# Performance work log

Hardware: AMD Instinct MI355X
Metric: run time of the kernel (lower is better)

The kernel has to match this reference:

```python
import jax, jax.numpy as jnp
import numpy as np

N = 50000
E = 800000
IN_C = 256
OUT_C = 256
HEADS = 8
HEAD_C = OUT_C // HEADS  # 32
BNECK = OUT_C // 4       # 64
NEG_SLOPE = 0.2
BN_EPS = 1e-5


def _bn(x, gamma, beta):
    # BatchNorm1d over node dim, batch statistics (deterministic train-mode math)
    mu = jnp.mean(x, axis=0)
    var = jnp.var(x, axis=0)
    return (x - mu) * jax.lax.rsqrt(var + BN_EPS) * gamma + beta


def setup_inputs() -> dict:
    key = jax.random.key(0)
    ks = jax.random.split(key, 16)
    s = lambda fan: 1.0 / np.sqrt(fan)
    x = jax.random.normal(ks[0], (N, IN_C), dtype=jnp.float32)
    edge_index = jax.random.randint(ks[1], (2, E), 0, N, dtype=jnp.int64)
    return {
        "x": x,
        "edge_index": edge_index,
        # GATConv params (lin has no bias in PyG)
        "W_lin": jax.random.normal(ks[2], (IN_C, HEADS * HEAD_C), jnp.float32) * s(IN_C),
        "att_src": jax.random.normal(ks[3], (HEADS, HEAD_C), jnp.float32) * s(HEAD_C),
        "att_dst": jax.random.normal(ks[4], (HEADS, HEAD_C), jnp.float32) * s(HEAD_C),
        "conv_bias": jnp.zeros((HEADS * HEAD_C,), jnp.float32),
        "W_res": jax.random.normal(ks[5], (IN_C, HEADS * HEAD_C), jnp.float32) * s(IN_C),
        # gnn.BatchNorm
        "g_norm": jnp.ones((OUT_C,), jnp.float32),
        "b_norm": jnp.zeros((OUT_C,), jnp.float32),
        # Bottleneck down
        "W_down": jax.random.normal(ks[6], (OUT_C, BNECK), jnp.float32) * s(OUT_C),
        "b_down": jnp.zeros((BNECK,), jnp.float32),
        "g_down": jnp.ones((BNECK,), jnp.float32),
        "bb_down": jnp.zeros((BNECK,), jnp.float32),
        # Bottleneck up
        "W_up": jax.random.normal(ks[7], (BNECK, OUT_C), jnp.float32) * s(BNECK),
        "b_up": jnp.zeros((OUT_C,), jnp.float32),
        "g_up": jnp.ones((OUT_C,), jnp.float32),
        "bb_up": jnp.zeros((OUT_C,), jnp.float32),
    }


def _forward(x, edge_index, W_lin, att_src, att_dst, conv_bias, W_res,
             g_norm, b_norm, W_down, b_down, g_down, bb_down,
             W_up, b_up, g_up, bb_up):
    src, dst = edge_index[0], edge_index[1]
    # --- GATConv ---
    xh = (x @ W_lin).reshape(N, HEADS, HEAD_C)            # [N,H,C]
    a_src = jnp.einsum("nhc,hc->nh", xh, att_src)          # [N,H]
    a_dst = jnp.einsum("nhc,hc->nh", xh, att_dst)          # [N,H]
    e = a_src[src] + a_dst[dst]                             # [E,H]
    e = jnp.where(e > 0, e, NEG_SLOPE * e)                  # leaky_relu
    # segment softmax over destination nodes (numerically stable)
    m = jax.ops.segment_max(e, dst, num_segments=N)         # [N,H]
    m = jnp.where(jnp.isfinite(m), m, 0.0)
    ex = jnp.exp(e - m[dst])
    denom = jax.ops.segment_sum(ex, dst, num_segments=N)    # [N,H]
    alpha = ex / (denom[dst] + 1e-16)                        # [E,H]
    msgs = xh[src] * alpha[:, :, None]                       # [E,H,C]
    out = jax.ops.segment_sum(msgs, dst, num_segments=N)    # [N,H,C]
    out = out.reshape(N, HEADS * HEAD_C) + conv_bias + x @ W_res  # GAT residual + bias
    # --- norm + act ---
    h = jax.nn.elu(_bn(out, g_norm, b_norm))
    # --- bottleneck ---
    d = jax.nn.elu(_bn(h @ W_down + b_down, g_down, bb_down))
    u = jax.nn.elu(_bn(d @ W_up + b_up, g_up, bb_up))
    h = h + u
    # dropout: eval mode (identity); in==out so identity skip
    return h + x


def reference(x, edge_index, W_lin, att_src, att_dst, conv_bias, W_res,
              g_norm, b_norm, W_down, b_down, g_down, bb_down,
              W_up, b_up, g_up, bb_up):
    return _forward(x, edge_index, W_lin, att_src, att_dst, conv_bias, W_res,
                    g_norm, b_norm, W_down, b_down, g_down, bb_down,
                    W_up, b_up, g_up, bb_up)
```

## Files before the change

### kernel.cpp

```cpp
#include <hip/hip_runtime.h>

#define NN 50000
#define EE 800000
#define HEADS 8
#define NEG 0.2f
#define BN_EPS 1e-5f
#define SCAN_B 196

typedef unsigned int uint;
typedef unsigned short ushort;

typedef __bf16 bf16x8 __attribute__((ext_vector_type(8)));
typedef float f32x4 __attribute__((ext_vector_type(4)));

__device__ __forceinline__ float bflo(uint u) { return __uint_as_float(u << 16); }
__device__ __forceinline__ float bfhi(uint u) { return __uint_as_float(u & 0xffff0000u); }
__device__ __forceinline__ float bf1(ushort u) { return __uint_as_float(((uint)u) << 16); }
__device__ __forceinline__ ushort f2bf(float f) {
  uint u = __float_as_uint(f);
  u += 0x7fff + ((u >> 16) & 1);
  return (ushort)(u >> 16);
}
__device__ __forceinline__ uint pk2(float a, float b) {
  return (uint)f2bf(a) | ((uint)f2bf(b) << 16);
}
__device__ __forceinline__ float eluf(float v) { return v > 0.f ? v : expm1f(v); }

__device__ __forceinline__ int blk_detect_bf16(const uint* __restrict__ xw) {
  __shared__ int s_bf;
  int t = threadIdx.x;
  if (t < 64) {
    int good = 0;
#pragma unroll
    for (int j = 0; j < 4; ++j) {
      uint lo = xw[t * 4 + j] & 0xffffu;
      uint ex = (lo >> 7) & 0xffu;
      good += (ex >= 110u && ex <= 140u) ? 1 : 0;
    }
    for (int o = 32; o; o >>= 1) good += __shfl_down(good, o);
    if (t == 0) s_bf = (good >= 128) ? 1 : 0;
  }
  __syncthreads();
  return s_bf;
}

__device__ __forceinline__ int blk_detect_i64(const int* __restrict__ ew) {
  __shared__ int s_i64;
  int t = threadIdx.x;
  if (t < 64) {
    int zeros = 0;
#pragma unroll
    for (int j = 0; j < 4; ++j)
      zeros += (ew[2 * (t * 4 + j) + 1] == 0) ? 1 : 0;
    for (int o = 32; o; o >>= 1) zeros += __shfl_down(zeros, o);
    if (t == 0) s_i64 = (zeros >= 200) ? 1 : 0;
  }
  __syncthreads();
  return s_i64;
}

__global__ __launch_bounds__(256)
void k_prep(const void* __restrict__ x,
            const void* p0, const void* p1, const void* p2, const void* p3,
            const void* p4, const void* p5, const void* p6, const void* p7,
            const void* p8, const void* p9, const void* p10,
            const void* W_lin, const void* W_res, const void* W_down, const void* W_up,
            float* __restrict__ P, ushort* __restrict__ bt1,
            ushort* __restrict__ bt2, ushort* __restrict__ bt3) {
  __shared__ ushort tile[64][65];
  int bf = blk_detect_bf16((const uint*)x);
  int b = blockIdx.x, t = threadIdx.x;
  if (b < 11) {
    const void* srcs[11] = {p0, p1, p2, p3, p4, p5, p6, p7, p8, p9, p10};
    const int sz[11]  = {256, 256, 256, 256, 256, 64, 64, 64, 256, 256, 256};
    const int off[11] = {0, 256, 512, 768, 1024, 1280, 1344, 1408, 1472, 1728, 1984};
    if (t < sz[b]) {
      const void* s = srcs[b];
      P[off[b] + t] = bf ? bf1(((const ushort*)s)[t]) : ((const float*)s)[t];
    }
    return;
  }
  const void* src; ushort* dst; int R, C, D, rb, cb;
  if (b < 27)      { int u = b - 11; src = W_lin;  dst = bt1;         R = 256; C = 256; D = 256; rb = u & 3; cb = u >> 2; }
  else if (b < 43) { int u = b - 27; src = W_res;  dst = bt1 + 65536; R = 256; C = 256; D = 256; rb = u & 3; cb = u >> 2; }
  else if (b < 51) { int u = b - 43; src = W_down; dst = bt2;         R = 256; C = 64;  D = 128; rb = u & 3; cb = u >> 2; }
  else             { int u = b - 51; src = W_up;   dst = bt3;         R = 64;  C = 256; D = 256; rb = 0;     cb = u; }
  int r0 = rb * 64, c0 = cb * 64;
  int tr = t >> 6, tc = t & 63;
#pragma unroll
  for (int i = 0; i < 16; ++i) {
    int rl = tr + i * 4;
    int r = r0 + rl, c = c0 + tc;
    float v = 0.f;
    if (r < R && c < C)
      v = bf ? bf1(((const ushort*)src)[(size_t)r * C + c])
             : ((const float*)src)[(size_t)r * C + c];
    tile[rl][tc] = f2bf(v);
  }
  __syncthreads();
#pragma unroll
  for (int i = 0; i < 16; ++i) {
    int cl = tr + i * 4;
    int rl = tc;
    int c = c0 + cl, r = r0 + rl;
    if (c < D && r < R)
      dst[(size_t)c * R + r] = (c < C) ? tile[rl][cl] : (ushort)0;
  }
}

__global__ __launch_bounds__(256)
void k_edges(const int* __restrict__ raw, int* __restrict__ sc, int* __restrict__ dc,
             int* __restrict__ count) {
  int i64 = blk_detect_i64(raw);
  int e = blockIdx.x * 256 + threadIdx.x;
  if (e >= EE) return;
  int s, d;
  if (i64) { s = raw[2 * e]; d = raw[2 * (EE + e)]; }
  else     { s = raw[e];     d = raw[EE + e]; }
  if ((uint)s >= NN) s = 0;
  if ((uint)d >= NN) d = 0;
  sc[e] = s; dc[e] = d;
  atomicAdd(&count[d], 1);
}

__global__ __launch_bounds__(256)
void k_gemm(const void* __restrict__ A, const ushort* __restrict__ Bt,
            int aMode, int nIter, int M, int K, int mode,
            ushort* __restrict__ o_xh, ushort* __restrict__ o_xres,
            ushort* __restrict__ o_bf, int NC, const float* __restrict__ bias,
            const float* __restrict__ bnsums, const float* __restrict__ bng,
            const float* __restrict__ bnb) {
  __shared__ __align__(16) ushort As[128 * 32];
  __shared__ __align__(16) ushort Bs[128 * 32];
  __shared__ float scs[256], shs[256];
  int t = threadIdx.x;
  int l = t & 63, w = t >> 6;
  int wr = w >> 1, wc = w & 1;
  int lr = l & 15, lq = l >> 4;
  int m0 = blockIdx.x * 128;
  const ushort* Ab = (const ushort*)A;
  const float*  Af = (const float*)A;

  int af32 = 0;
  if (aMode == 1) af32 = blk_detect_bf16((const uint*)A) ? 0 : 1;
  if (aMode == 2) {
    if (t < K) {
      const float invN = 1.0f / NN;
      float mean = bnsums[t] * invN;
      float var = bnsums[K + t] * invN - mean * mean;
      float sc = bng[t] * rsqrtf(var + BN_EPS);
      scs[t] = sc;
      shs[t] = bnb[t] - mean * sc;
    }
  }

  for (int nc = 0; nc < nIter; ++nc) {
    int n0 = nc * 128;
    f32x4 acc[4][4];
#pragma unroll
    for (int i = 0; i < 4; ++i)
#pragma unroll
      for (int j = 0; j < 4; ++j) acc[i][j] = (f32x4){0.f, 0.f, 0.f, 0.f};

    for (int kt = 0; kt < K; kt += 32) {
      __syncthreads();
#pragma unroll
      for (int r = 0; r < 2; ++r) {
        int ci = r * 256 + t;
        int m = ci >> 2, ko = (ci & 3) << 3;
        int gm = m0 + m; gm = gm < M ? gm : M - 1;
        if (aMode == 1 && af32) {
          float4 u0 = *(const float4*)(Af + (size_t)gm * K + kt + ko);
          float4 u1 = *(const float4*)(Af + (size_t)gm * K + kt + ko + 4);
          uint4 o;
          o.x = pk2(u0.x, u0.y); o.y = pk2(u0.z, u0.w);
          o.z = pk2(u1.x, u1.y); o.w = pk2(u1.z, u1.w);
          *(uint4*)(&As[m * 32 + ko]) = o;
        } else if (aMode == 2) {
          uint4 q = *(const uint4*)(Ab + (size_t)gm * K + kt + ko);
          int cb = kt + ko;
          float v0 = eluf(bflo(q.x) * scs[cb + 0] + shs[cb + 0]);
          float v1 = eluf(bfhi(q.x) * scs[cb + 1] + shs[cb + 1]);
          float v2 = eluf(bflo(q.y) * scs[cb + 2] + shs[cb + 2]);
          float v3 = eluf(bfhi(q.y) * scs[cb + 3] + shs[cb + 3]);
          float v4 = eluf(bflo(q.z) * scs[cb + 4] + shs[cb + 4]);
          float v5 = eluf(bfhi(q.z) * scs[cb + 5] + shs[cb + 5]);
          float v6 = eluf(bflo(q.w) * scs[cb + 6] + shs[cb + 6]);
          float v7 = eluf(bfhi(q.w) * scs[cb + 7] + shs[cb + 7]);
          uint4 o;
          o.x = pk2(v0, v1); o.y = pk2(v2, v3);
          o.z = pk2(v4, v5); o.w = pk2(v6, v7);
          *(uint4*)(&As[m * 32 + ko]) = o;
        } else {
          *(uint4*)(&As[m * 32 + ko]) = *(const uint4*)(Ab + (size_t)gm * K + kt + ko);
        }
        *(uint4*)(&Bs[m * 32 + ko]) = *(const uint4*)(Bt + (size_t)(n0 + m) * K + kt + ko);
      }
      __syncthreads();
      bf16x8 af[4], bf[4];
#pragma unroll
      for (int i = 0; i < 4; ++i) {
        af[i] = *(const bf16x8*)(&As[(wr * 64 + i * 16 + lr) * 32 + lq * 8]);
        bf[i] = *(const bf16x8*)(&Bs[(wc * 64 + i * 16 + lr) * 32 + lq * 8]);
      }
#pragma unroll
      for (int i = 0; i < 4; ++i)
#pragma unroll
        for (int j = 0; j < 4; ++j)
          acc[i][j] = __builtin_amdgcn_mfma_f32_16x16x32_bf16(af[i], bf[j], acc[i][j], 0, 0, 0);
    }

#pragma unroll
    for (int i = 0; i < 4; ++i) {
      int gr0 = m0 + wr * 64 + i * 16 + lq * 4;
#pragma unroll
      for (int j = 0; j < 4; ++j) {
        int gc = n0 + wc * 64 + j * 16 + lr;
#pragma unroll
        for (int r = 0; r < 4; ++r) {
          int row = gr0 + r;
          if (row >= M) continue;
          float v = acc[i][j][r];
          if (mode == 0) {
            if (gc < 256) o_xh[(size_t)row * 256 + gc] = f2bf(v);
            else          o_xres[(size_t)row * 256 + (gc - 256)] = f2bf(v);
          } else {
            if (gc < NC) o_bf[(size_t)row * NC + gc] = f2bf(v + bias[gc]);
          }
        }
      }
    }
  }
}

__global__ void k_attn(const ushort* __restrict__ xh, const float* __restrict__ P,
                       float* __restrict__ a_src, float* __restrict__ a_dst) {
  int id = blockIdx.x * 256 + threadIdx.x;
  if (id >= NN * HEADS) return;
  int n = id >> 3, h = id & 7;
  const uint4* xr = (const uint4*)(xh + (size_t)n * 256 + h * 32);
  const float4* pa = (const float4*)(P + h * 32);
  const float4* pd = (const float4*)(P + 256 + h * 32);
  float s = 0.f, d = 0.f;
#pragma unroll
  for (int j = 0; j < 4; ++j) {
    uint4 q = xr[j];
    float4 a0 = pa[2 * j], a1 = pa[2 * j + 1];
    float4 d0 = pd[2 * j], d1 = pd[2 * j + 1];
    float x0 = bflo(q.x), x1 = bfhi(q.x), x2 = bflo(q.y), x3 = bfhi(q.y);
    float x4 = bflo(q.z), x5 = bfhi(q.z), x6 = bflo(q.w), x7 = bfhi(q.w);
    s += x0 * a0.x + x1 * a0.y + x2 * a0.z + x3 * a0.w
       + x4 * a1.x + x5 * a1.y + x6 * a1.z + x7 * a1.w;
    d += x0 * d0.x + x1 * d0.y + x2 * d0.z + x3 * d0.w
       + x4 * d1.x + x5 * d1.y + x6 * d1.z + x7 * d1.w;
  }
  a_src[id] = s; a_dst[id] = d;
}

__global__ void k_scan_bs(const int* __restrict__ count, int* __restrict__ bsum) {
  __shared__ int s[256];
  int i = blockIdx.x * 256 + threadIdx.x;
  s[threadIdx.x] = (i < NN) ? count[i] : 0;
  __syncthreads();
  for (int off = 128; off > 0; off >>= 1) {
    if (threadIdx.x < off) s[threadIdx.x] += s[threadIdx.x + off];
    __syncthreads();
  }
  if (threadIdx.x == 0) bsum[blockIdx.x] = s[0];
}

__global__ void k_scan_top(const int* __restrict__ bsum, int* __restrict__ boff,
                           int* __restrict__ rowptr) {
  __shared__ int s[256];
  int t = threadIdx.x;
  int v = (t < SCAN_B) ? bsum[t] : 0;
  s[t] = v;
  __syncthreads();
  for (int off = 1; off < 256; off <<= 1) {
    int u = (t >= off) ? s[t - off] : 0;
    __syncthreads();
    s[t] += u;
    __syncthreads();
  }
  boff[t] = s[t] - v;
  if (t == 255) rowptr[NN] = s[255];
}

__global__ void k_scan_wr(const int* __restrict__ count, const int* __restrict__ boff,
                          int* __restrict__ rowptr, int* __restrict__ rowwork) {
  __shared__ int s[256];
  int b = blockIdx.x, t = threadIdx.x;
  int i = b * 256 + t;
  int v = (i < NN) ? count[i] : 0;
  s[t] = v;
  __syncthreads();
  for (int off = 1; off < 256; off <<= 1) {
    int u = (t >= off) ? s[t - off] : 0;
    __syncthreads();
    s[t] += u;
    __syncthreads();
  }
  if (i < NN) {
    int ex = boff[b] + s[t] - v;
    rowptr[i] = ex;
    rowwork[i] = ex;
  }
}

__global__ void k_scatter(const int* __restrict__ sc, const int* __restrict__ dc,
                          int* __restrict__ rowwork, int* __restrict__ perm_src) {
  int e = blockIdx.x * 256 + threadIdx.x;
  if (e >= EE) return;
  int pos = atomicAdd(&rowwork[dc[e]], 1);
  perm_src[pos] = sc[e];
}

__global__ __launch_bounds__(256)
void k_aggregate(const int* __restrict__ rowptr, const int* __restrict__ perm_src,
                 const float* __restrict__ a_src, const float* __restrict__ a_dst,
                 const ushort* __restrict__ xh, const ushort* __restrict__ xres,
                 const float* __restrict__ bias, ushort* __restrict__ outb) {
  int n = blockIdx.x * 4 + (threadIdx.x >> 6);
  int l = threadIdx.x & 63;
  if (n >= NN) return;
  int half = l >> 5;
  int q = l & 31;
  int h = q >> 2;
  float ad = a_dst[n * 8 + h];
  int st = rowptr[n], en = rowptr[n + 1];
  float a0 = 0.f, a1 = 0.f, a2 = 0.f, a3 = 0.f;
  float a4 = 0.f, a5 = 0.f, a6 = 0.f, a7 = 0.f, sum = 0.f;
  int p = st + half;
  int s_c = 0; float e_c = 0.f; uint4 x_c = {0, 0, 0, 0};
  if (p < en) {
    s_c = perm_src[p];
    e_c = a_src[s_c * 8 + h];
    x_c = *(const uint4*)(xh + (size_t)s_c * 256 + q * 8);
  }
  for (; p < en; p += 2) {
    int pn = p + 2;
    int s_n = 0; float e_n = 0.f; uint4 x_n = {0, 0, 0, 0};
    if (pn < en) {
      s_n = perm_src[pn];
      e_n = a_src[s_n * 8 + h];
      x_n = *(const uint4*)(xh + (size_t)s_n * 256 + q * 8);
    }
    float v = e_c + ad;
    v = v > 0.f ? v : NEG * v;
    float wgt = __expf(fminf(v, 60.f));
    sum += wgt;
    a0 += wgt * bflo(x_c.x); a1 += wgt * bfhi(x_c.x);
    a2 += wgt * bflo(x_c.y); a3 += wgt * bfhi(x_c.y);
    a4 += wgt * bflo(x_c.z); a5 += wgt * bfhi(x_c.z);
    a6 += wgt * bflo(x_c.w); a7 += wgt * bfhi(x_c.w);
    s_c = s_n; e_c = e_n; x_c = x_n;
  }
  sum += __shfl_xor(sum, 32);
  a0 += __shfl_xor(a0, 32); a1 += __shfl_xor(a1, 32);
  a2 += __shfl_xor(a2, 32); a3 += __shfl_xor(a3, 32);
  a4 += __shfl_xor(a4, 32); a5 += __shfl_xor(a5, 32);
  a6 += __shfl_xor(a6, 32); a7 += __shfl_xor(a7, 32);
  if (half == 0) {
    float inv = 1.0f / (sum + 1e-16f);
    int cb = q * 8;
    float4 b0 = *(const float4*)(bias + cb);
    float4 b1 = *(const float4*)(bias + cb + 4);
    uint4 qr = *(const uint4*)(xres + (size_t)n * 256 + cb);
    uint4 pk;
    pk.x = pk2(a0 * inv + b0.x + bflo(qr.x), a1 * inv + b0.y + bfhi(qr.x));
    pk.y = pk2(a2 * inv + b0.z + bflo(qr.y), a3 * inv + b0.w + bfhi(qr.y));
    pk.z = pk2(a4 * inv + b1.x + bflo(qr.z), a5 * inv + b1.y + bfhi(qr.z));
    pk.w = pk2(a6 * inv + b1.z + bflo(qr.w), a7 * inv + b1.w + bfhi(qr.w));
    *(uint4*)(outb + (size_t)n * 256 + cb) = pk;
  }
}

__global__ __launch_bounds__(256)
void k_stats_p(const ushort* __restrict__ x, float* __restrict__ sums, int n, int C) {
  __shared__ float4 redA[256];
  __shared__ float4 redB[256];
  int t = threadIdx.x, b = blockIdx.x;
  int W = C >> 2;
  int c4 = t & (W - 1);
  int rl = t / W;
  int G = 256 / W;
  int rows = (n + 63) / 64;
  int r0 = b * rows, r1 = r0 + rows; if (r1 > n) r1 = n;
  const uint2* xu = (const uint2*)x;
  float s0 = 0, s1 = 0, s2 = 0, s3 = 0, q0 = 0, q1 = 0, q2 = 0, q3 = 0;
  for (int r = r0 + rl; r < r1; r += G) {
    uint2 v = xu[(size_t)r * W + c4];
    float v0 = bflo(v.x), v1 = bfhi(v.x), v2 = bflo(v.y), v3 = bfhi(v.y);
    s0 += v0; s1 += v1; s2 += v2; s3 += v3;
    q0 += v0 * v0; q1 += v1 * v1; q2 += v2 * v2; q3 += v3 * v3;
  }
  redA[t] = make_float4(s0, s1, s2, s3);
  redB[t] = make_float4(q0, q1, q2, q3);
  __syncthreads();
  for (int off = 128; off >= W; off >>= 1) {
    if (t < off) {
      float4 a = redA[t + off], c = redA[t];
      redA[t] = make_float4(c.x + a.x, c.y + a.y, c.z + a.z, c.w + a.w);
      float4 d = redB[t + off], e = redB[t];
      redB[t] = make_float4(e.x + d.x, e.y + d.y, e.z + d.z, e.w + d.w);
    }
    __syncthreads();
  }
  if (t < W) {
    float4 a = redA[t], d = redB[t];
    atomicAdd(&sums[4 * c4 + 0], a.x); atomicAdd(&sums[4 * c4 + 1], a.y);
    atomicAdd(&sums[4 * c4 + 2], a.z); atomicAdd(&sums[4 * c4 + 3], a.w);
    atomicAdd(&sums[C + 4 * c4 + 0], d.x); atomicAdd(&sums[C + 4 * c4 + 1], d.y);
    atomicAdd(&sums[C + 4 * c4 + 2], d.z); atomicAdd(&sums[C + 4 * c4 + 3], d.w);
  }
}

__global__ void k_final(const ushort* __restrict__ upre, const float* __restrict__ sums3,
                        const ushort* __restrict__ og, const float* __restrict__ sums1,
                        const float* __restrict__ P, const void* __restrict__ xsrc,
                        void* __restrict__ outv) {
  int bf = blk_detect_bf16((const uint*)xsrc);
  int id = blockIdx.x * 256 + threadIdx.x;
  size_t base = (size_t)id * 4;
  if (base >= (size_t)NN * 256) return;
  int c = (int)(base & 255);
  const float invN = 1.0f / NN;
  float4 s3m = *(const float4*)(sums3 + c);
  float4 s3q = *(const float4*)(sums3 + 256 + c);
  float4 g3 = *(const float4*)(P + 1728 + c);
  float4 b3 = *(const float4*)(P + 1984 + c);
  float4 s1m = *(const float4*)(sums1 + c);
  float4 s1q = *(const float4*)(sums1 + 256 + c);
  float4 g1 = *(const float4*)(P + 768 + c);
  float4 b1 = *(const float4*)(P + 1024 + c);
  uint2 qu = *(const uint2*)(upre + base);
  uint2 qo = *(const uint2*)(og + base);
  float xv[4];
  if (bf) {
    uint2 qx = *(const uint2*)((const ushort*)xsrc + base);
    xv[0] = bflo(qx.x); xv[1] = bfhi(qx.x); xv[2] = bflo(qx.y); xv[3] = bfhi(qx.y);
  } else {
    float4 qx = *(const float4*)((const float*)xsrc + base);
    xv[0] = qx.x; xv[1] = qx.y; xv[2] = qx.z; xv[3] = qx.w;
  }
  float uv[4] = {bflo(qu.x), bfhi(qu.x), bflo(qu.y), bfhi(qu.y)};
  float ov[4] = {bflo(qo.x), bfhi(qo.x), bflo(qo.y), bfhi(qo.y)};
  float s3mv[4] = {s3m.x, s3m.y, s3m.z, s3m.w}, s3qv[4] = {s3q.x, s3q.y, s3q.z, s3q.w};
  float g3v[4] = {g3.x, g3.y, g3.z, g3.w}, b3v[4] = {b3.x, b3.y, b3.z, b3.w};
  float s1mv[4] = {s1m.x, s1m.y, s1m.z, s1m.w}, s1qv[4] = {s1q.x, s1q.y, s1q.z, s1q.w};
  float g1v[4] = {g1.x, g1.y, g1.z, g1.w}, b1v[4] = {b1.x, b1.y, b1.z, b1.w};
  float o[4];
#pragma unroll
  for (int j = 0; j < 4; ++j) {
    float m3 = s3mv[j] * invN;
    float v3 = s3qv[j] * invN - m3 * m3;
    float sc3 = g3v[j] * rsqrtf(v3 + BN_EPS);
    float u = eluf((uv[j] - m3) * sc3 + b3v[j]);
    float m1 = s1mv[j] * invN;
    float v1 = s1qv[j] * invN - m1 * m1;
    float sc1 = g1v[j] * rsqrtf(v1 + BN_EPS);
    float h1 = eluf((ov[j] - m1) * sc1 + b1v[j]);
    o[j] = u + h1 + xv[j];
  }
  if (bf) {
    uint2 pk;
    pk.x = pk2(o[0], o[1]);
    pk.y = pk2(o[2], o[3]);
    *(uint2*)((ushort*)outv + base) = pk;
  } else {
    *(float4*)((float*)outv + base) = make_float4(o[0], o[1], o[2], o[3]);
  }
}

extern "C" void kernel_launch(void* const* d_in, const int* in_sizes, int n_in,
                              void* d_out, int out_size, void* d_ws, size_t ws_size,
                              hipStream_t stream) {
  const void* x      = d_in[0];
  const int*  ei     = (const int*)d_in[1];
  const void* W_lin  = d_in[2];
  const void* att_s  = d_in[3];
  const void* att_d  = d_in[4];
  const void* c_bias = d_in[5];
  const void* W_res  = d_in[6];
  const void* g_norm = d_in[7];
  const void* b_norm = d_in[8];
  const void* W_down = d_in[9];
  const void* b_down = d_in[10];
  const void* g_down = d_in[11];
  const void* bb_down= d_in[12];
  const void* W_up   = d_in[13];
  const void* b_up   = d_in[14];
  const void* g_up   = d_in[15];
  const void* bb_up  = d_in[16];

  char* ws = (char*)d_ws;
  size_t off = 0;
  auto alloc = [&](size_t bytes) -> char* {
    char* p = ws + off;
    off = (off + bytes + 255) & ~(size_t)255;
    return p;
  };
  int*   count  = (int*)alloc((size_t)NN * 4);
  float* sums1  = (float*)alloc(512 * 4);
  float* sums2  = (float*)alloc(128 * 4);
  float* sums3  = (float*)alloc(512 * 4);
  size_t zbytes = off;
  float* P      = (float*)alloc(2240 * 4);
  int* bsum     = (int*)alloc(256 * 4);
  int* boff     = (int*)alloc(256 * 4);
  int* rowptr   = (int*)alloc((size_t)(NN + 1) * 4);
  int* rowwork  = (int*)alloc((size_t)(NN + 1) * 4);
  int* src_c    = (int*)alloc((size_t)EE * 4);
  int* dst_c    = (int*)alloc((size_t)EE * 4);
  int* perm_src = (int*)alloc((size_t)EE * 4);
  ushort* bt1   = (ushort*)alloc((size_t)512 * 256 * 2);
  ushort* bt2   = (ushort*)alloc((size_t)128 * 256 * 2);
  ushort* bt3   = (ushort*)alloc((size_t)256 * 64 * 2);
  float* a_src  = (float*)alloc((size_t)NN * 8 * 4);
  float* a_dst  = (float*)alloc((size_t)NN * 8 * 4);
  ushort* xh    = (ushort*)alloc((size_t)NN * 256 * 2);
  ushort* xres  = (ushort*)alloc((size_t)NN * 256 * 2);
  ushort* og_b  = (ushort*)alloc((size_t)NN * 256 * 2);
  ushort* d_pre_b = xh;
  ushort* u_pre_b = xres;

  hipMemsetAsync(d_ws, 0, zbytes, stream);

  hipLaunchKernelGGL(k_prep, dim3(55), dim3(256), 0, stream, x,
                     att_s, att_d, c_bias, g_norm, b_norm, b_down, g_down, bb_down,
                     b_up, g_up, bb_up, W_lin, W_res, W_down, W_up, P, bt1, bt2, bt3);
  hipLaunchKernelGGL(k_edges, dim3((EE + 255) / 256), dim3(256), 0, stream,
                     ei, src_c, dst_c, count);

  hipLaunchKernelGGL(k_gemm, dim3(391), dim3(256), 0, stream, x, bt1, 1, 4,
                     NN, 256, 0, xh, xres, (ushort*)nullptr, 0,
                     (const float*)nullptr, (const float*)nullptr,
                     (const float*)nullptr, (const float*)nullptr);
  hipLaunchKernelGGL(k_attn, dim3((NN * 8 + 255) / 256), dim3(256), 0, stream,
                     xh, P, a_src, a_dst);

  hipLaunchKernelGGL(k_scan_bs, dim3(SCAN_B), dim3(256), 0, stream, count, bsum);
  hipLaunchKernelGGL(k_scan_top, dim3(1), dim3(256), 0, stream, bsum, boff, rowptr);
  hipLaunchKernelGGL(k_scan_wr, dim3(SCAN_B), dim3(256), 0, stream, count, boff, rowptr, rowwork);
  hipLaunchKernelGGL(k_scatter, dim3((EE + 255) / 256), dim3(256), 0, stream,
                     src_c, dst_c, rowwork, perm_src);

  hipLaunchKernelGGL(k_aggregate, dim3(NN / 4), dim3(256), 0, stream, rowptr, perm_src,
                     a_src, a_dst, xh, xres, P + 512, og_b);

  hipLaunchKernelGGL(k_stats_p, dim3(64), dim3(256), 0, stream, og_b, sums1, NN, 256);

  hipLaunchKernelGGL(k_gemm, dim3(391), dim3(256), 0, stream, og_b, bt2, 2, 1,
                     NN, 256, 1, (ushort*)nullptr, (ushort*)nullptr, d_pre_b, 64,
                     P + 1280, sums1, P + 768, P + 1024);
  hipLaunchKernelGGL(k_stats_p, dim3(64), dim3(256), 0, stream, d_pre_b, sums2, NN, 64);

  hipLaunchKernelGGL(k_gemm, dim3(391), dim3(256), 0, stream, d_pre_b, bt3, 2, 2,
                     NN, 64, 1, (ushort*)nullptr, (ushort*)nullptr, u_pre_b, 256,
                     P + 1472, sums2, P + 1344, P + 1408);
  hipLaunchKernelGGL(k_stats_p, dim3(64), dim3(256), 0, stream, u_pre_b, sums3, NN, 256);

  hipLaunchKernelGGL(k_final, dim3(NN * 256 / 4 / 256), dim3(256), 0, stream,
                     u_pre_b, sums3, og_b, sums1, P, x, d_out);
}
```

Measured before the change: 621.3 us.

## Stage full A row-tile in padded LDS once and read B directly from global

The GEMM kernel now loads the block's whole 128xK A tile into dynamic shared memory once, padded by 8 elements per row to avoid bank conflicts, with the BN+ELU prologue applied during that load. It then reuses the tile across all N-chunks instead of re-staging A for every chunk. B fragments are read straight from global memory (cached) inside the K loop, which removes the per-iteration barriers and B staging. The cost is larger LDS use (about 66 KB for K=256), which can lower occupancy, plus uncoalesced per-lane global B loads.

```diff
diff --git a/kernel.cpp b/kernel.cpp
--- a/kernel.cpp
+++ b/kernel.cpp
@@ -130,29 +130,60 @@
             ushort* __restrict__ o_bf, int NC, const float* __restrict__ bias,
             const float* __restrict__ bnsums, const float* __restrict__ bng,
             const float* __restrict__ bnb) {
-  __shared__ __align__(16) ushort As[128 * 32];
-  __shared__ __align__(16) ushort Bs[128 * 32];
+  extern __shared__ __align__(16) ushort Asl[];
   __shared__ float scs[256], shs[256];
   int t = threadIdx.x;
   int l = t & 63, w = t >> 6;
   int wr = w >> 1, wc = w & 1;
   int lr = l & 15, lq = l >> 4;
   int m0 = blockIdx.x * 128;
+  int stride = K + 8;
   const ushort* Ab = (const ushort*)A;
   const float*  Af = (const float*)A;
 
+  if (aMode == 2 && t < K) {
+    const float invN = 1.0f / NN;
+    float mean = bnsums[t] * invN;
+    float var = bnsums[K + t] * invN - mean * mean;
+    float sc = bng[t] * rsqrtf(var + BN_EPS);
+    scs[t] = sc;
+    shs[t] = bnb[t] - mean * sc;
+  }
+  __syncthreads();
   int af32 = 0;
   if (aMode == 1) af32 = blk_detect_bf16((const uint*)A) ? 0 : 1;
-  if (aMode == 2) {
-    if (t < K) {
-      const float invN = 1.0f / NN;
-      float mean = bnsums[t] * invN;
-      float var = bnsums[K + t] * invN - mean * mean;
-      float sc = bng[t] * rsqrtf(var + BN_EPS);
-      scs[t] = sc;
-      shs[t] = bnb[t] - mean * sc;
-    }
-  }
+
+  int W = K >> 3;
+  int total = 128 * W;
+  for (int ci = t; ci < total; ci += 256) {
+    int m = ci / W, ko = (ci - m * W) * 8;
+    int gm = m0 + m; gm = gm < M ? gm : M - 1;
+    uint4 o;
+    if (aMode == 1 && af32) {
+      float4 u0 = *(const float4*)(Af + (size_t)gm * K + ko);
+      float4 u1 = *(const float4*)(Af + (size_t)gm * K + ko + 4);
+      o.x = pk2(u0.x, u0.y); o.y = pk2(u0.z, u0.w);
+      o.z = pk2(u1.x, u1.y); o.w = pk2(u1.z, u1.w);
+    } else {
+      uint4 q = *(const uint4*)(Ab + (size_t)gm * K + ko);
+      if (aMode == 2) {
+        float v0 = eluf(bflo(q.x) * scs[ko + 0] + shs[ko + 0]);
+        float v1 = eluf(bfhi(q.x) * scs[ko + 1] + shs[ko + 1]);
+        float v2 = eluf(bflo(q.y) * scs[ko + 2] + shs[ko + 2]);
+        float v3 = eluf(bfhi(q.y) * scs[ko + 3] + shs[ko + 3]);
+        float v4 = eluf(bflo(q.z) * scs[ko + 4] + shs[ko + 4]);
+        float v5 = eluf(bfhi(q.z) * scs[ko + 5] + shs[ko + 5]);
+        float v6 = eluf(bflo(q.w) * scs[ko + 6] + shs[ko + 6]);
+        float v7 = eluf(bfhi(q.w) * scs[ko + 7] + shs[ko + 7]);
+        o.x = pk2(v0, v1); o.y = pk2(v2, v3);
+        o.z = pk2(v4, v5); o.w = pk2(v6, v7);
+      } else {
+        o = q;
+      }
+    }
+    *(uint4*)(&Asl[m * stride + ko]) = o;
+  }
+  __syncthreads();
 
   for (int nc = 0; nc < nIter; ++nc) {
     int n0 = nc * 128;
@@ -162,47 +193,17 @@
 #pragma unroll
       for (int j = 0; j < 4; ++j) acc[i][j] = (f32x4){0.f, 0.f, 0.f, 0.f};
 
+    const ushort* bbase = Bt + (size_t)(n0 + wc * 64 + lr) * K + lq * 8;
+    const ushort* arow = &Asl[(wr * 64 + lr) * stride + lq * 8];
+
     for (int kt = 0; kt < K; kt += 32) {
-      __syncthreads();
-#pragma unroll
-      for (int r = 0; r < 2; ++r) {
-        int ci = r * 256 + t;
-        int m = ci >> 2, ko = (ci & 3) << 3;
-        int gm = m0 + m; gm = gm < M ? gm : M - 1;
-        if (aMode == 1 && af32) {
-          float4 u0 = *(const float4*)(Af + (size_t)gm * K + kt + ko);
-          float4 u1 = *(const float4*)(Af + (size_t)gm * K + kt + ko + 4);
-          uint4 o;
-          o.x = pk2(u0.x, u0.y); o.y = pk2(u0.z, u0.w);
-          o.z = pk2(u1.x, u1.y); o.w = pk2(u1.z, u1.w);
-          *(uint4*)(&As[m * 32 + ko]) = o;
-        } else if (aMode == 2) {
-          uint4 q = *(const uint4*)(Ab + (size_t)gm * K + kt + ko);
-          int cb = kt + ko;
-          float v0 = eluf(bflo(q.x) * scs[cb + 0] + shs[cb + 0]);
-          float v1 = eluf(bfhi(q.x) * scs[cb + 1] + shs[cb + 1]);
-          float v2 = eluf(bflo(q.y) * scs[cb + 2] + shs[cb + 2]);
-          float v3 = eluf(bfhi(q.y) * scs[cb + 3] + shs[cb + 3]);
-          float v4 = eluf(bflo(q.z) * scs[cb + 4] + shs[cb + 4]);
-          float v5 = eluf(bfhi(q.z) * scs[cb + 5] + shs[cb + 5]);
-          float v6 = eluf(bflo(q.w) * scs[cb + 6] + shs[cb + 6]);
-          float v7 = eluf(bfhi(q.w) * scs[cb + 7] + shs[cb + 7]);
-          uint4 o;
-          o.x = pk2(v0, v1); o.y = pk2(v2, v3);
-          o.z = pk2(v4, v5); o.w = pk2(v6, v7);
-          *(uint4*)(&As[m * 32 + ko]) = o;
-        } else {
-          *(uint4*)(&As[m * 32 + ko]) = *(const uint4*)(Ab + (size_t)gm * K + kt + ko);
-        }
-        *(uint4*)(&Bs[m * 32 + ko]) = *(const uint4*)(Bt + (size_t)(n0 + m) * K + kt + ko);
-      }
-      __syncthreads();
       bf16x8 af[4], bf[4];
 #pragma unroll
-      for (int i = 0; i < 4; ++i) {
-        af[i] = *(const bf16x8*)(&As[(wr * 64 + i * 16 + lr) * 32 + lq * 8]);
-        bf[i] = *(const bf16x8*)(&Bs[(wc * 64 + i * 16 + lr) * 32 + lq * 8]);
-      }
+      for (int i = 0; i < 4; ++i)
+        af[i] = *(const bf16x8*)(arow + i * 16 * stride + kt);
+#pragma unroll
+      for (int i = 0; i < 4; ++i)
+        bf[i] = *(const bf16x8*)(bbase + (size_t)i * 16 * K + kt);
 #pragma unroll
       for (int i = 0; i < 4; ++i)
 #pragma unroll
@@ -532,7 +533,10 @@
   hipLaunchKernelGGL(k_edges, dim3((EE + 255) / 256), dim3(256), 0, stream,
                      ei, src_c, dst_c, count);
 
-  hipLaunchKernelGGL(k_gemm, dim3(391), dim3(256), 0, stream, x, bt1, 1, 4,
+  const size_t lds256 = 128 * (256 + 8) * 2;
+  const size_t lds64  = 128 * (64 + 8) * 2;
+
+  hipLaunchKernelGGL(k_gemm, dim3(391), dim3(256), lds256, stream, x, bt1, 1, 4,
                      NN, 256, 0, xh, xres, (ushort*)nullptr, 0,
                      (const float*)nullptr, (const float*)nullptr,
                      (const float*)nullptr, (const float*)nullptr);
@@ -550,12 +554,12 @@
 
   hipLaunchKernelGGL(k_stats_p, dim3(64), dim3(256), 0, stream, og_b, sums1, NN, 256);
 
-  hipLaunchKernelGGL(k_gemm, dim3(391), dim3(256), 0, stream, og_b, bt2, 2, 1,
+  hipLaunchKernelGGL(k_gemm, dim3(391), dim3(256), lds256, stream, og_b, bt2, 2, 1,
                      NN, 256, 1, (ushort*)nullptr, (ushort*)nullptr, d_pre_b, 64,
                      P + 1280, sums1, P + 768, P + 1024);
   hipLaunchKernelGGL(k_stats_p, dim3(64), dim3(256), 0, stream, d_pre_b, sums2, NN, 64);
 
-  hipLaunchKernelGGL(k_gemm, dim3(391), dim3(256), 0, stream, d_pre_b, bt3, 2, 2,
+  hipLaunchKernelGGL(k_gemm, dim3(391), dim3(256), lds64, stream, d_pre_b, bt3, 2, 2,
                      NN, 64, 1, (ushort*)nullptr, (ushort*)nullptr, u_pre_b, 256,
                      P + 1472, sums2, P + 1344, P + 1408);
   hipLaunchKernelGGL(k_stats_p, dim3(64), dim3(256), 0, stream, u_pre_b, sums3, NN, 256);
```

Result: no change. 610.2 us (-1.8%).
